# Optimization experiments

Hardware: AMD Instinct MI355X
Metric: run time of the kernel (lower is better)

The kernel has to match this reference:

```python
import jax, jax.numpy as jnp
import numpy as np

TOP_K = 2  # num_experts_per_tok


def setup_inputs() -> dict:
    key = jax.random.key(0)
    ks = jax.random.split(key, 4)
    B, S, H, I, E = 4, 2048, 2048, 4096, 8
    std = 0.02
    hidden_states = jax.random.normal(ks[0], (B, S, H), dtype=jnp.float32)
    gate_w = jax.random.normal(ks[1], (E, H), dtype=jnp.float32) * std   # nn.Linear weight [E,H]
    wfc = jax.random.normal(ks[2], (E, I, H), dtype=jnp.float32) * std   # c_fc weight [E,out,in]
    bfc = jnp.zeros((E, I), dtype=jnp.float32)                           # bias zero-init
    wproj = jax.random.normal(ks[3], (E, H, I), dtype=jnp.float32) * std # c_proj weight
    bproj = jnp.zeros((E, H), dtype=jnp.float32)
    return {"hidden_states": hidden_states, "gate_w": gate_w, "wfc": wfc,
            "bfc": bfc, "wproj": wproj, "bproj": bproj}


def reference(hidden_states, gate_w, wfc, bfc, wproj, bproj):
    B, S, H = hidden_states.shape
    E = wfc.shape[0]
    x = hidden_states.reshape(-1, H)                      # [T, H]
    router_logits = x @ gate_w.T                          # [T, E]
    top_vals, top_idx = jax.lax.top_k(router_logits, TOP_K)
    router_weights = jax.nn.softmax(top_vals.astype(jnp.float32), axis=-1).astype(x.dtype)  # [T, k]
    out = jnp.zeros_like(x)
    # Loop over the small fixed set of experts; each token contributes with its
    # combined gate weight for that expert (0 if not routed there). Same math as
    # the torch gather/grouped-GEMM/scatter-add path.
    for e in range(E):
        gate_e = jnp.sum(jnp.where(top_idx == e, router_weights, 0.0), axis=-1)  # [T]
        h = jax.nn.gelu(x @ wfc[e].T + bfc[e], approximate=False)                # [T, I]
        y = h @ wproj[e].T + bproj[e]                                            # [T, H]
        out = out + gate_e[:, None] * y
    return out.reshape(B, S, H), router_logits
```

## Files before the change

kernel.cpp:

```cpp
#include <hip/hip_runtime.h>
#include <hip/hip_bf16.h>
#include <math.h>

#define NT 8192
#define HD 2048
#define ID 4096
#define NE 8
#define MAXSLOT 18432
#define MAXRB 72

typedef __bf16 bf16x8 __attribute__((ext_vector_type(8)));
typedef float f32x4 __attribute__((ext_vector_type(4)));

__device__ __forceinline__ float bf2f(unsigned short u){
  union{unsigned u; float f;} v; v.u = ((unsigned)u) << 16; return v.f;
}

__device__ __forceinline__ void gload_lds16(const void* g, void* l){
  __builtin_amdgcn_global_load_lds((const __attribute__((address_space(1))) void*)g,
                                   (__attribute__((address_space(3))) void*)l, 16, 0, 0);
}

__global__ __launch_bounds__(256) void cvt_kernel(const float* __restrict__ in,
                                                  __hip_bfloat16* __restrict__ outp, int n4){
  int i = blockIdx.x * blockDim.x + threadIdx.x;
  int stride = gridDim.x * blockDim.x;
  for (; i < n4; i += stride){
    float4 v = reinterpret_cast<const float4*>(in)[i];
    union{ushort4 u; __hip_bfloat16 h[4];} o;
    o.h[0] = __float2bfloat16(v.x); o.h[1] = __float2bfloat16(v.y);
    o.h[2] = __float2bfloat16(v.z); o.h[3] = __float2bfloat16(v.w);
    reinterpret_cast<ushort4*>(outp)[i] = o.u;
  }
}

__global__ __launch_bounds__(256) void router_kernel(
    const float* __restrict__ x, const float* __restrict__ gw,
    float* __restrict__ logits_out, int* __restrict__ tokExp,
    float* __restrict__ tokW, int* __restrict__ cnt)
{
  int wave = (blockIdx.x * blockDim.x + threadIdx.x) >> 6;
  int lane = threadIdx.x & 63;
  if (wave >= NT) return;
  const float* xr = x + (long)wave * HD;
  double acc[NE];
  #pragma unroll
  for (int e = 0; e < NE; e++) acc[e] = 0.0;
  for (int k = lane; k < HD; k += 64){
    double xv = (double)xr[k];
    #pragma unroll
    for (int e = 0; e < NE; e++) acc[e] += xv * (double)gw[e * HD + k];
  }
  #pragma unroll
  for (int e = 0; e < NE; e++){
    #pragma unroll
    for (int off = 32; off; off >>= 1) acc[e] += __shfl_down(acc[e], off, 64);
  }
  if (lane == 0){
    int e0 = 0; double v0 = acc[0];
    for (int e = 1; e < NE; e++) if (acc[e] > v0){ v0 = acc[e]; e0 = e; }
    int e1 = -1; double v1 = -1e300;
    for (int e = 0; e < NE; e++) if (e != e0 && acc[e] > v1){ v1 = acc[e]; e1 = e; }
    double ex = exp(v1 - v0);
    double s = 1.0 + ex;
    for (int e = 0; e < NE; e++) logits_out[wave * NE + e] = (float)acc[e];
    tokExp[wave * 2]     = e0; tokExp[wave * 2 + 1] = e1;
    tokW[wave * 2]       = (float)(1.0 / s);
    tokW[wave * 2 + 1]   = (float)(ex / s);
    atomicAdd(&cnt[e0], 1); atomicAdd(&cnt[e1], 1);
  }
}

__global__ void offsets_kernel(const int* __restrict__ cnt, int* __restrict__ padOff){
  if (threadIdx.x == 0 && blockIdx.x == 0){
    int o = 0;
    for (int e = 0; e < NE; e++){ padOff[e] = o; o += ((cnt[e] + 255) >> 8) << 8; }
    padOff[NE] = o;
  }
}

__global__ __launch_bounds__(256) void scatter_kernel(
    const int* __restrict__ tokExp, const int* __restrict__ padOff, int* cursor,
    int* __restrict__ slotTok)
{
  int t = blockIdx.x * blockDim.x + threadIdx.x;
  if (t >= NT) return;
  #pragma unroll
  for (int s = 0; s < 2; s++){
    int e = tokExp[t * 2 + s];
    int pos = atomicAdd(&cursor[e], 1);
    slotTok[padOff[e] + pos] = t * 2 + s;
  }
}


#define LDA(buf,kk,m) (*reinterpret_cast<const bf16x8*>(&lds[((buf)*2+(kk))*8192 + (wr*8+(m))*512 + laneF]))
#define LDB(buf,kk,n) (*reinterpret_cast<const bf16x8*>(&lds[32768 + ((buf)*2+(kk))*8192 + (wc*4+(n))*512 + laneF]))
#define STAGE_A(buf,kk,koff) do{ \
    __hip_bfloat16* d_ = &lds[((buf)*2+(kk))*8192 + w*1024]; \
    gload_lds16(aS0 + (koff), d_); \
    gload_lds16(aS1 + (koff), d_ + 512); \
  }while(0)
#define STAGE_B(buf,kk,koff) do{ \
    __hip_bfloat16* d_ = &lds[32768 + ((buf)*2+(kk))*8192 + w*1024]; \
    gload_lds16(bS0 + (koff), d_); \
    gload_lds16(bS1 + (koff), d_ + 512); \
  }while(0)
#define MFMA16(M0,A0_,A1_,A2_,A3_) do{ \
    acc[(M0)+0][0] = __builtin_amdgcn_mfma_f32_16x16x32_bf16(A0_, bv0, acc[(M0)+0][0],0,0,0); \
    acc[(M0)+1][0] = __builtin_amdgcn_mfma_f32_16x16x32_bf16(A1_, bv0, acc[(M0)+1][0],0,0,0); \
    acc[(M0)+2][0] = __builtin_amdgcn_mfma_f32_16x16x32_bf16(A2_, bv0, acc[(M0)+2][0],0,0,0); \
    acc[(M0)+3][0] = __builtin_amdgcn_mfma_f32_16x16x32_bf16(A3_, bv0, acc[(M0)+3][0],0,0,0); \
    acc[(M0)+0][1] = __builtin_amdgcn_mfma_f32_16x16x32_bf16(A0_, bv1, acc[(M0)+0][1],0,0,0); \
    acc[(M0)+1][1] = __builtin_amdgcn_mfma_f32_16x16x32_bf16(A1_, bv1, acc[(M0)+1][1],0,0,0); \
    acc[(M0)+2][1] = __builtin_amdgcn_mfma_f32_16x16x32_bf16(A2_, bv1, acc[(M0)+2][1],0,0,0); \
    acc[(M0)+3][1] = __builtin_amdgcn_mfma_f32_16x16x32_bf16(A3_, bv1, acc[(M0)+3][1],0,0,0); \
    acc[(M0)+0][2] = __builtin_amdgcn_mfma_f32_16x16x32_bf16(A0_, bv2, acc[(M0)+0][2],0,0,0); \
    acc[(M0)+1][2] = __builtin_amdgcn_mfma_f32_16x16x32_bf16(A1_, bv2, acc[(M0)+1][2],0,0,0); \
    acc[(M0)+2][2] = __builtin_amdgcn_mfma_f32_16x16x32_bf16(A2_, bv2, acc[(M0)+2][2],0,0,0); \
    acc[(M0)+3][2] = __builtin_amdgcn_mfma_f32_16x16x32_bf16(A3_, bv2, acc[(M0)+3][2],0,0,0); \
    acc[(M0)+0][3] = __builtin_amdgcn_mfma_f32_16x16x32_bf16(A0_, bv3, acc[(M0)+0][3],0,0,0); \
    acc[(M0)+1][3] = __builtin_amdgcn_mfma_f32_16x16x32_bf16(A1_, bv3, acc[(M0)+1][3],0,0,0); \
    acc[(M0)+2][3] = __builtin_amdgcn_mfma_f32_16x16x32_bf16(A2_, bv3, acc[(M0)+3][3],0,0,0); \
    acc[(M0)+3][3] = __builtin_amdgcn_mfma_f32_16x16x32_bf16(A3_, bv3, acc[(M0)+3][3],0,0,0); \
  }while(0)

#undef MFMA16
#define MFMA16(M0,A0_,A1_,A2_,A3_) do{ \
    acc[(M0)+0][0] = __builtin_amdgcn_mfma_f32_16x16x32_bf16(A0_, bv0, acc[(M0)+0][0],0,0,0); \
    acc[(M0)+1][0] = __builtin_amdgcn_mfma_f32_16x16x32_bf16(A1_, bv0, acc[(M0)+1][0],0,0,0); \
    acc[(M0)+2][0] = __builtin_amdgcn_mfma_f32_16x16x32_bf16(A2_, bv0, acc[(M0)+2][0],0,0,0); \
    acc[(M0)+3][0] = __builtin_amdgcn_mfma_f32_16x16x32_bf16(A3_, bv0, acc[(M0)+3][0],0,0,0); \
    acc[(M0)+0][1] = __builtin_amdgcn_mfma_f32_16x16x32_bf16(A0_, bv1, acc[(M0)+0][1],0,0,0); \
    acc[(M0)+1][1] = __builtin_amdgcn_mfma_f32_16x16x32_bf16(A1_, bv1, acc[(M0)+1][1],0,0,0); \
    acc[(M0)+2][1] = __builtin_amdgcn_mfma_f32_16x16x32_bf16(A2_, bv1, acc[(M0)+2][1],0,0,0); \
    acc[(M0)+3][1] = __builtin_amdgcn_mfma_f32_16x16x32_bf16(A3_, bv1, acc[(M0)+3][1],0,0,0); \
    acc[(M0)+0][2] = __builtin_amdgcn_mfma_f32_16x16x32_bf16(A0_, bv2, acc[(M0)+0][2],0,0,0); \
    acc[(M0)+1][2] = __builtin_amdgcn_mfma_f32_16x16x32_bf16(A1_, bv2, acc[(M0)+1][2],0,0,0); \
    acc[(M0)+2][2] = __builtin_amdgcn_mfma_f32_16x16x32_bf16(A2_, bv2, acc[(M0)+2][2],0,0,0); \
    acc[(M0)+3][2] = __builtin_amdgcn_mfma_f32_16x16x32_bf16(A3_, bv2, acc[(M0)+3][2],0,0,0); \
    acc[(M0)+0][3] = __builtin_amdgcn_mfma_f32_16x16x32_bf16(A0_, bv3, acc[(M0)+0][3],0,0,0); \
    acc[(M0)+1][3] = __builtin_amdgcn_mfma_f32_16x16x32_bf16(A1_, bv3, acc[(M0)+1][3],0,0,0); \
    acc[(M0)+2][3] = __builtin_amdgcn_mfma_f32_16x16x32_bf16(A2_, bv3, acc[(M0)+2][3],0,0,0); \
    acc[(M0)+3][3] = __builtin_amdgcn_mfma_f32_16x16x32_bf16(A3_, bv3, acc[(M0)+3][3],0,0,0); \
  }while(0)

template<int GDIV, int EPI, int ND, int KD>
__global__ __launch_bounds__(512, 2) void moe_gemm8(
    const __hip_bfloat16* __restrict__ A,
    const __hip_bfloat16* __restrict__ W,
    const float* __restrict__ bias,
    const int* __restrict__ slotTok,
    const int* __restrict__ padOff,
    __hip_bfloat16* __restrict__ Yout)
{
  __shared__ __align__(16) __hip_bfloat16 lds[65536];
  const int rb = blockIdx.y;
  if (rb * 256 >= padOff[NE]) return;
  const int cb = blockIdx.x;
  int e = 0;
  #pragma unroll
  for (int i = 1; i < NE; i++) if (rb * 256 >= padOff[i]) e = i;

  const int tid  = threadIdx.x;
  const int lane = tid & 63;
  const int w    = tid >> 6;
  const int wr   = w >> 2;
  const int wc   = w & 3;

  const int r16s = lane >> 2;
  const int cgs  = (lane & 3) ^ ((r16s >> 1) & 3);
  const int rowA = rb * 256 + 32 * w + r16s;
  int pr0 = slotTok[rowA];      long ga0 = pr0 < 0 ? 0 : (pr0 >> GDIV);
  int pr1 = slotTok[rowA + 16]; long ga1 = pr1 < 0 ? 0 : (pr1 >> GDIV);
  const __hip_bfloat16* aS0 = A + ga0 * (long)KD + cgs * 8;
  const __hip_bfloat16* aS1 = A + ga1 * (long)KD + cgs * 8;
  const long rowB = (long)cb * 256 + 32 * w + r16s;
  const __hip_bfloat16* bS0 = W + (long)e * ND * KD + rowB * KD + cgs * 8;
  const __hip_bfloat16* bS1 = bS0 + 16 * (long)KD;

  const int r16f = lane & 15;
  const int chf  = lane >> 4;
  const int laneF = r16f * 32 + (chf ^ ((r16f >> 1) & 3)) * 8;

  f32x4 acc[8][4] = {};
  bf16x8 bv0, bv1, bv2, bv3;

  constexpr int NTILES = KD / 64;

  STAGE_A(0,0,0);   STAGE_B(0,0,0);
  STAGE_A(0,1,32);  STAGE_B(0,1,32);
  STAGE_A(1,0,64);  STAGE_B(1,0,64);
  STAGE_A(1,1,96);  STAGE_B(1,1,96);
  asm volatile("s_waitcnt vmcnt(8)" ::: "memory");
  __builtin_amdgcn_s_barrier();

  for (int t = 0; t < NTILES; ++t){
    const int b = t & 1;
    const bool s01 = (t >= 1) && (t + 1 < NTILES);
    const bool s23 = (t + 2 < NTILES);
    const long ko01 = (long)(t + 1) * 64 + 32;
    const long ko23 = (long)(t + 2) * 64;
    {
      bf16x8 a0 = LDA(b,0,0), a1 = LDA(b,0,1), a2 = LDA(b,0,2), a3 = LDA(b,0,3);
      bv0 = LDB(b,0,0); bv1 = LDB(b,0,1); bv2 = LDB(b,0,2); bv3 = LDB(b,0,3);
      if (s01){ STAGE_A(b^1,1,ko01); }
      __builtin_amdgcn_s_barrier();
      asm volatile("s_waitcnt lgkmcnt(0)" ::: "memory");
      __builtin_amdgcn_s_setprio(1);
      MFMA16(0, a0, a1, a2, a3);
      __builtin_amdgcn_s_setprio(0);
      __builtin_amdgcn_s_barrier();
    }
    {
      bf16x8 a0 = LDA(b,0,4), a1 = LDA(b,0,5), a2 = LDA(b,0,6), a3 = LDA(b,0,7);
      if (s01){ STAGE_B(b^1,1,ko01); }
      __builtin_amdgcn_s_barrier();
      asm volatile("s_waitcnt lgkmcnt(0)" ::: "memory");
      __builtin_amdgcn_s_setprio(1);
      MFMA16(4, a0, a1, a2, a3);
      __builtin_amdgcn_s_setprio(0);
      __builtin_amdgcn_s_barrier();
    }
    {
      bf16x8 a0 = LDA(b,1,0), a1 = LDA(b,1,1), a2 = LDA(b,1,2), a3 = LDA(b,1,3);
      bv0 = LDB(b,1,0); bv1 = LDB(b,1,1); bv2 = LDB(b,1,2); bv3 = LDB(b,1,3);
      if (s23){ STAGE_A(b,0,ko23); }
      __builtin_amdgcn_s_barrier();
      asm volatile("s_waitcnt lgkmcnt(0)" ::: "memory");
      __builtin_amdgcn_s_setprio(1);
      MFMA16(0, a0, a1, a2, a3);
      __builtin_amdgcn_s_setprio(0);
      __builtin_amdgcn_s_barrier();
    }
    {
      bf16x8 a0 = LDA(b,1,4), a1 = LDA(b,1,5), a2 = LDA(b,1,6), a3 = LDA(b,1,7);
      if (s23){ STAGE_B(b,0,ko23); }
      __builtin_amdgcn_s_barrier();
      asm volatile("s_waitcnt lgkmcnt(0)" ::: "memory");
      __builtin_amdgcn_s_setprio(1);
      MFMA16(4, a0, a1, a2, a3);
      __builtin_amdgcn_s_setprio(0);
      if (s23) asm volatile("s_waitcnt vmcnt(4)" ::: "memory");
      else     asm volatile("s_waitcnt vmcnt(0)" ::: "memory");
      __builtin_amdgcn_s_barrier();
    }
  }

  const int colBase = cb * 256 + wc * 64 + (lane & 15);
  const int rowQ = (lane >> 4) * 4;
  float bb[4];
  #pragma unroll
  for (int n = 0; n < 4; n++) bb[n] = bias[(long)e * ND + colBase + n * 16];
  #pragma unroll
  for (int m = 0; m < 8; m++){
    const int grow = rb * 256 + wr * 128 + m * 16 + rowQ;
    #pragma unroll
    for (int r = 0; r < 4; r++){
      const int pr = slotTok[grow + r];
      if (pr >= 0){
        #pragma unroll
        for (int n = 0; n < 4; n++){
          float v = acc[m][n][r] + bb[n];
          if (EPI == 0){
            v = 0.5f * v * (1.0f + erff(v * 0.70710678118654752f));
          }
          Yout[(long)pr * ND + colBase + n * 16] = __float2bfloat16(v);
        }
      }
    }
  }
}

__global__ __launch_bounds__(256) void combine_kernel(
    const __hip_bfloat16* __restrict__ yb, const float* __restrict__ tokW,
    float* __restrict__ outp)
{
  const int t  = blockIdx.x;
  const int c0 = threadIdx.x * 8;
  const float w0 = tokW[t * 2], w1 = tokW[t * 2 + 1];
  const ushort4* p0 = reinterpret_cast<const ushort4*>(yb + (long)(2 * t) * HD + c0);
  const ushort4* p1 = reinterpret_cast<const ushort4*>(yb + (long)(2 * t + 1) * HD + c0);
  float4 o[2];
  #pragma unroll
  for (int h = 0; h < 2; h++){
    ushort4 a = p0[h], b = p1[h];
    o[h].x = w0 * bf2f(a.x) + w1 * bf2f(b.x);
    o[h].y = w0 * bf2f(a.y) + w1 * bf2f(b.y);
    o[h].z = w0 * bf2f(a.z) + w1 * bf2f(b.z);
    o[h].w = w0 * bf2f(a.w) + w1 * bf2f(b.w);
  }
  float4* po = reinterpret_cast<float4*>(outp + (long)t * HD + c0);
  po[0] = o[0]; po[1] = o[1];
}

extern "C" void kernel_launch(void* const* d_in, const int* in_sizes, int n_in,
                              void* d_out, int out_size, void* d_ws, size_t ws_size,
                              hipStream_t stream)
{
  (void)in_sizes; (void)n_in; (void)out_size; (void)ws_size;
  const float* x     = (const float*)d_in[0];
  const float* gw    = (const float*)d_in[1];
  const float* wfc   = (const float*)d_in[2];
  const float* bfc   = (const float*)d_in[3];
  const float* wproj = (const float*)d_in[4];
  const float* bproj = (const float*)d_in[5];
  float* outp   = (float*)d_out;
  float* logits = outp + (size_t)NT * HD;

  char* ws = (char*)d_ws;
  size_t off = 0;
  auto alloc = [&](size_t b){ void* p = ws + off; off += (b + 255) & ~(size_t)255; return p; };

  char* region0 = (char*)alloc((size_t)NT * 2 * HD * 2);
  __hip_bfloat16* xb = (__hip_bfloat16*)region0;
  __hip_bfloat16* yb = (__hip_bfloat16*)region0;
  __hip_bfloat16* hb = (__hip_bfloat16*)alloc((size_t)NT * 2 * ID * 2);
  __hip_bfloat16* wB = (__hip_bfloat16*)alloc((size_t)NE * ID * HD * 2);
  int*   slotTok = (int*)alloc(MAXSLOT * 4);
  int*   tokExp  = (int*)alloc(NT * 2 * 4);
  float* tokW    = (float*)alloc(NT * 2 * 4);
  int*   meta    = (int*)alloc(256);
  int* cnt = meta; int* cursor = meta + 8; int* padOff = meta + 16;

  hipMemsetAsync(meta, 0, 256, stream);
  hipMemsetAsync(slotTok, 0xFF, MAXSLOT * 4, stream);

  cvt_kernel<<<2048, 256, 0, stream>>>(x, xb, NT * HD / 4);
  router_kernel<<<NT / 4, 256, 0, stream>>>(x, gw, logits, tokExp, tokW, cnt);
  offsets_kernel<<<1, 64, 0, stream>>>(cnt, padOff);
  scatter_kernel<<<NT / 256, 256, 0, stream>>>(tokExp, padOff, cursor, slotTok);

  cvt_kernel<<<2048, 256, 0, stream>>>(wfc, wB, NE * ID * HD / 4);
  moe_gemm8<1, 0, ID, HD><<<dim3(ID / 256, MAXRB), 512, 0, stream>>>(xb, wB, bfc, slotTok, padOff, hb);
  cvt_kernel<<<2048, 256, 0, stream>>>(wproj, wB, NE * HD * ID / 4);
  moe_gemm8<0, 1, HD, ID><<<dim3(HD / 256, MAXRB), 512, 0, stream>>>(hb, wB, bproj, slotTok, padOff, yb);

  combine_kernel<<<NT, 256, 0, stream>>>(yb, tokW, outp);
}
```

Measured before the change: 1.230 ms.

## Gather tokens into slot-ordered bf16 buffer so MoE GEMMs read rows contiguously

A new gather-convert kernel copies each routed token's activations into a slot-contiguous bf16 buffer. The first GEMM then reads A rows contiguously and writes the intermediate activations in slot order. The second GEMM reads those rows contiguously and scatters its output only at the epilogue. The bf16 expert outputs are now staged in the output buffer and combined in place, with a block barrier so each row is read before it is overwritten. The goal is to replace indirect row gathers in the GEMM loads with sequential access. In exchange it costs an extra gather pass over padded slots and a larger workspace, with a fallback to the old path when the workspace is too small.

```diff
diff --git a/kernel.cpp b/kernel.cpp
--- a/kernel.cpp
+++ b/kernel.cpp
@@ -32,6 +32,30 @@
     o.h[2] = __float2bfloat16(v.z); o.h[3] = __float2bfloat16(v.w);
     reinterpret_cast<ushort4*>(outp)[i] = o.u;
   }
+}
+
+__global__ __launch_bounds__(256) void gather_cvt_kernel(
+    const float* __restrict__ x, const int* __restrict__ slotTok,
+    __hip_bfloat16* __restrict__ xg)
+{
+  const int slot = blockIdx.x;
+  const int c = threadIdx.x * 8;
+  const int pr = slotTok[slot];
+  ushort4* dst = reinterpret_cast<ushort4*>(xg + (long)slot * HD + c);
+  if (pr < 0){
+    ushort4 z = {0,0,0,0};
+    dst[0] = z; dst[1] = z;
+    return;
+  }
+  const float* src = x + (long)(pr >> 1) * HD + c;
+  float4 v0 = reinterpret_cast<const float4*>(src)[0];
+  float4 v1 = reinterpret_cast<const float4*>(src)[1];
+  union{ushort4 u; __hip_bfloat16 h[4];} a, b;
+  a.h[0]=__float2bfloat16(v0.x); a.h[1]=__float2bfloat16(v0.y);
+  a.h[2]=__float2bfloat16(v0.z); a.h[3]=__float2bfloat16(v0.w);
+  b.h[0]=__float2bfloat16(v1.x); b.h[1]=__float2bfloat16(v1.y);
+  b.h[2]=__float2bfloat16(v1.z); b.h[3]=__float2bfloat16(v1.w);
+  dst[0] = a.u; dst[1] = b.u;
 }
 
 __global__ __launch_bounds__(256) void router_kernel(
@@ -121,31 +145,11 @@
     acc[(M0)+3][2] = __builtin_amdgcn_mfma_f32_16x16x32_bf16(A3_, bv2, acc[(M0)+3][2],0,0,0); \
     acc[(M0)+0][3] = __builtin_amdgcn_mfma_f32_16x16x32_bf16(A0_, bv3, acc[(M0)+0][3],0,0,0); \
     acc[(M0)+1][3] = __builtin_amdgcn_mfma_f32_16x16x32_bf16(A1_, bv3, acc[(M0)+1][3],0,0,0); \
-    acc[(M0)+2][3] = __builtin_amdgcn_mfma_f32_16x16x32_bf16(A2_, bv3, acc[(M0)+3][3],0,0,0); \
-    acc[(M0)+3][3] = __builtin_amdgcn_mfma_f32_16x16x32_bf16(A3_, bv3, acc[(M0)+3][3],0,0,0); \
-  }while(0)
-
-#undef MFMA16
-#define MFMA16(M0,A0_,A1_,A2_,A3_) do{ \
-    acc[(M0)+0][0] = __builtin_amdgcn_mfma_f32_16x16x32_bf16(A0_, bv0, acc[(M0)+0][0],0,0,0); \
-    acc[(M0)+1][0] = __builtin_amdgcn_mfma_f32_16x16x32_bf16(A1_, bv0, acc[(M0)+1][0],0,0,0); \
-    acc[(M0)+2][0] = __builtin_amdgcn_mfma_f32_16x16x32_bf16(A2_, bv0, acc[(M0)+2][0],0,0,0); \
-    acc[(M0)+3][0] = __builtin_amdgcn_mfma_f32_16x16x32_bf16(A3_, bv0, acc[(M0)+3][0],0,0,0); \
-    acc[(M0)+0][1] = __builtin_amdgcn_mfma_f32_16x16x32_bf16(A0_, bv1, acc[(M0)+0][1],0,0,0); \
-    acc[(M0)+1][1] = __builtin_amdgcn_mfma_f32_16x16x32_bf16(A1_, bv1, acc[(M0)+1][1],0,0,0); \
-    acc[(M0)+2][1] = __builtin_amdgcn_mfma_f32_16x16x32_bf16(A2_, bv1, acc[(M0)+2][1],0,0,0); \
-    acc[(M0)+3][1] = __builtin_amdgcn_mfma_f32_16x16x32_bf16(A3_, bv1, acc[(M0)+3][1],0,0,0); \
-    acc[(M0)+0][2] = __builtin_amdgcn_mfma_f32_16x16x32_bf16(A0_, bv2, acc[(M0)+0][2],0,0,0); \
-    acc[(M0)+1][2] = __builtin_amdgcn_mfma_f32_16x16x32_bf16(A1_, bv2, acc[(M0)+1][2],0,0,0); \
-    acc[(M0)+2][2] = __builtin_amdgcn_mfma_f32_16x16x32_bf16(A2_, bv2, acc[(M0)+2][2],0,0,0); \
-    acc[(M0)+3][2] = __builtin_amdgcn_mfma_f32_16x16x32_bf16(A3_, bv2, acc[(M0)+3][2],0,0,0); \
-    acc[(M0)+0][3] = __builtin_amdgcn_mfma_f32_16x16x32_bf16(A0_, bv3, acc[(M0)+0][3],0,0,0); \
-    acc[(M0)+1][3] = __builtin_amdgcn_mfma_f32_16x16x32_bf16(A1_, bv3, acc[(M0)+1][3],0,0,0); \
     acc[(M0)+2][3] = __builtin_amdgcn_mfma_f32_16x16x32_bf16(A2_, bv3, acc[(M0)+2][3],0,0,0); \
     acc[(M0)+3][3] = __builtin_amdgcn_mfma_f32_16x16x32_bf16(A3_, bv3, acc[(M0)+3][3],0,0,0); \
   }while(0)
 
-template<int GDIV, int EPI, int ND, int KD>
+template<int AGATHER, int WSC, int EPI, int ND, int KD>
 __global__ __launch_bounds__(512, 2) void moe_gemm8(
     const __hip_bfloat16* __restrict__ A,
     const __hip_bfloat16* __restrict__ W,
@@ -170,9 +174,15 @@
 
   const int r16s = lane >> 2;
   const int cgs  = (lane & 3) ^ ((r16s >> 1) & 3);
-  const int rowA = rb * 256 + 32 * w + r16s;
-  int pr0 = slotTok[rowA];      long ga0 = pr0 < 0 ? 0 : (pr0 >> GDIV);
-  int pr1 = slotTok[rowA + 16]; long ga1 = pr1 < 0 ? 0 : (pr1 >> GDIV);
+  const int r0 = rb * 256 + 32 * w + r16s;
+  long ga0, ga1;
+  if (AGATHER == 0){
+    ga0 = r0; ga1 = r0 + 16;
+  } else {
+    int p0 = slotTok[r0], p1 = slotTok[r0 + 16];
+    ga0 = p0 < 0 ? 0 : (AGATHER == 1 ? (p0 >> 1) : p0);
+    ga1 = p1 < 0 ? 0 : (AGATHER == 1 ? (p1 >> 1) : p1);
+  }
   const __hip_bfloat16* aS0 = A + ga0 * (long)KD + cgs * 8;
   const __hip_bfloat16* aS1 = A + ga1 * (long)KD + cgs * 8;
   const long rowB = (long)cb * 256 + 32 * w + r16s;
@@ -257,15 +267,18 @@
     const int grow = rb * 256 + wr * 128 + m * 16 + rowQ;
     #pragma unroll
     for (int r = 0; r < 4; r++){
-      const int pr = slotTok[grow + r];
-      if (pr >= 0){
+      long orow;
+      bool doW;
+      if (WSC == 0){ orow = grow + r; doW = true; }
+      else { int pr = slotTok[grow + r]; orow = pr; doW = (pr >= 0); }
+      if (doW){
         #pragma unroll
         for (int n = 0; n < 4; n++){
           float v = acc[m][n][r] + bb[n];
           if (EPI == 0){
             v = 0.5f * v * (1.0f + erff(v * 0.70710678118654752f));
           }
-          Yout[(long)pr * ND + colBase + n * 16] = __float2bfloat16(v);
+          Yout[orow * ND + colBase + n * 16] = __float2bfloat16(v);
         }
       }
     }
@@ -290,6 +303,7 @@
     o[h].z = w0 * bf2f(a.z) + w1 * bf2f(b.z);
     o[h].w = w0 * bf2f(a.w) + w1 * bf2f(b.w);
   }
+  __syncthreads();
   float4* po = reinterpret_cast<float4*>(outp + (long)t * HD + c0);
   po[0] = o[0]; po[1] = o[1];
 }
@@ -298,7 +312,7 @@
                               void* d_out, int out_size, void* d_ws, size_t ws_size,
                               hipStream_t stream)
 {
-  (void)in_sizes; (void)n_in; (void)out_size; (void)ws_size;
+  (void)in_sizes; (void)n_in; (void)out_size;
   const float* x     = (const float*)d_in[0];
   const float* gw    = (const float*)d_in[1];
   const float* wfc   = (const float*)d_in[2];
@@ -307,16 +321,28 @@
   const float* bproj = (const float*)d_in[5];
   float* outp   = (float*)d_out;
   float* logits = outp + (size_t)NT * HD;
+  __hip_bfloat16* yb = (__hip_bfloat16*)d_out;
 
   char* ws = (char*)d_ws;
   size_t off = 0;
   auto alloc = [&](size_t b){ void* p = ws + off; off += (b + 255) & ~(size_t)255; return p; };
 
-  char* region0 = (char*)alloc((size_t)NT * 2 * HD * 2);
-  __hip_bfloat16* xb = (__hip_bfloat16*)region0;
-  __hip_bfloat16* yb = (__hip_bfloat16*)region0;
-  __hip_bfloat16* hb = (__hip_bfloat16*)alloc((size_t)NT * 2 * ID * 2);
-  __hip_bfloat16* wB = (__hip_bfloat16*)alloc((size_t)NE * ID * HD * 2);
+  const size_t XG_B  = (size_t)MAXSLOT * HD * 2;
+  const size_t HBS_B = (size_t)MAXSLOT * ID * 2;
+  const size_t WB_B  = (size_t)NE * ID * HD * 2;
+  const size_t MISC_B = (size_t)MAXSLOT*4 + NT*2*4 + NT*2*4 + 4096;
+  const bool slotPath = (XG_B + HBS_B + WB_B + MISC_B + 4096) <= ws_size;
+
+  __hip_bfloat16 *xg, *hb, *wB;
+  if (slotPath){
+    xg = (__hip_bfloat16*)alloc(XG_B);
+    hb = (__hip_bfloat16*)alloc(HBS_B);
+    wB = (__hip_bfloat16*)alloc(WB_B);
+  } else {
+    xg = (__hip_bfloat16*)alloc((size_t)NT * HD * 2);
+    hb = (__hip_bfloat16*)alloc((size_t)NT * 2 * ID * 2);
+    wB = (__hip_bfloat16*)alloc(WB_B);
+  }
   int*   slotTok = (int*)alloc(MAXSLOT * 4);
   int*   tokExp  = (int*)alloc(NT * 2 * 4);
   float* tokW    = (float*)alloc(NT * 2 * 4);
@@ -326,15 +352,23 @@
   hipMemsetAsync(meta, 0, 256, stream);
   hipMemsetAsync(slotTok, 0xFF, MAXSLOT * 4, stream);
 
-  cvt_kernel<<<2048, 256, 0, stream>>>(x, xb, NT * HD / 4);
   router_kernel<<<NT / 4, 256, 0, stream>>>(x, gw, logits, tokExp, tokW, cnt);
   offsets_kernel<<<1, 64, 0, stream>>>(cnt, padOff);
   scatter_kernel<<<NT / 256, 256, 0, stream>>>(tokExp, padOff, cursor, slotTok);
 
-  cvt_kernel<<<2048, 256, 0, stream>>>(wfc, wB, NE * ID * HD / 4);
-  moe_gemm8<1, 0, ID, HD><<<dim3(ID / 256, MAXRB), 512, 0, stream>>>(xb, wB, bfc, slotTok, padOff, hb);
-  cvt_kernel<<<2048, 256, 0, stream>>>(wproj, wB, NE * HD * ID / 4);
-  moe_gemm8<0, 1, HD, ID><<<dim3(HD / 256, MAXRB), 512, 0, stream>>>(hb, wB, bproj, slotTok, padOff, yb);
+  if (slotPath){
+    gather_cvt_kernel<<<MAXSLOT, 256, 0, stream>>>(x, slotTok, xg);
+    cvt_kernel<<<2048, 256, 0, stream>>>(wfc, wB, NE * ID * HD / 4);
+    moe_gemm8<0, 0, 0, ID, HD><<<dim3(ID / 256, MAXRB), 512, 0, stream>>>(xg, wB, bfc, slotTok, padOff, hb);
+    cvt_kernel<<<2048, 256, 0, stream>>>(wproj, wB, NE * HD * ID / 4);
+    moe_gemm8<0, 1, 1, HD, ID><<<dim3(HD / 256, MAXRB), 512, 0, stream>>>(hb, wB, bproj, slotTok, padOff, yb);
+  } else {
+    cvt_kernel<<<2048, 256, 0, stream>>>(x, xg, NT * HD / 4);
+    cvt_kernel<<<2048, 256, 0, stream>>>(wfc, wB, NE * ID * HD / 4);
+    moe_gemm8<1, 1, 0, ID, HD><<<dim3(ID / 256, MAXRB), 512, 0, stream>>>(xg, wB, bfc, slotTok, padOff, hb);
+    cvt_kernel<<<2048, 256, 0, stream>>>(wproj, wB, NE * HD * ID / 4);
+    moe_gemm8<2, 1, 1, HD, ID><<<dim3(HD / 256, MAXRB), 512, 0, stream>>>(hb, wB, bproj, slotTok, padOff, yb);
+  }
 
   combine_kernel<<<NT, 256, 0, stream>>>(yb, tokW, outp);
 }
```

New measurement: 1.250 ms. Within noise of the previous version (+1.6%).
